# Kernel tuning notes

Hardware: AMD Instinct MI355X
Metric: run time of the kernel (lower is better)

The kernel has to match this reference:

```python
import jax, jax.numpy as jnp
import numpy as np

B, T, I, E, K, J = 4, 4096, 1024, 16, 512, 1024


def setup_inputs() -> dict:
    key = jax.random.key(0)
    k1, k2, k3 = jax.random.split(key, 3)
    X = jax.random.normal(k1, (B, T, I), dtype=jnp.float32)
    ind = jax.random.randint(k2, (B, E, K), 0, T, dtype=jnp.int64)
    bound = 1.0 / np.sqrt(J)
    W = jax.random.uniform(k3, (E, I, J), dtype=jnp.float32, minval=-bound, maxval=bound)
    return {"X": X, "ind": ind, "W": W}


def reference(X, ind, W):
    Bs, Ts, Is = X.shape
    _, Es, Ks = ind.shape
    # gather tokens per expert: [B, E*K, I] -> [B, E, K, I]
    idx = ind.reshape(Bs, Es * Ks)
    Xg = jnp.take_along_axis(X, idx[:, :, None], axis=1).reshape(Bs, Es, Ks, Is)
    # per-expert GEMM
    Y = jnp.einsum('beki,eij->bekj', Xg, W)
    return Y
```

## Files before the change

kernel.cpp:

```cpp
#include <hip/hip_runtime.h>
#include <cstdint>
#include <cstddef>


typedef float    floatx4 __attribute__((ext_vector_type(4)));
typedef _Float16 half8   __attribute__((ext_vector_type(8)));

constexpr int Bc = 4, Tc = 4096, Ic = 1024, Ec = 16, Kc = 512, Jc = 1024;
constexpr int BM = 256, BN = 256, BK = 64, NT = 512;

__device__ __forceinline__ void async16(const void* g, void* l) {
  __builtin_amdgcn_global_load_lds(
      (const __attribute__((address_space(1))) uint32_t*)g,
      (__attribute__((address_space(3))) uint32_t*)l, 16, 0, 0);
}

__global__ void cvt_x_kernel(const float* __restrict__ X, _Float16* __restrict__ Xh, int n8) {
  int i = blockIdx.x * blockDim.x + threadIdx.x;
  int stride = gridDim.x * blockDim.x;
  for (; i < n8; i += stride) {
    floatx4 v0 = ((const floatx4*)X)[2 * i];
    floatx4 v1 = ((const floatx4*)X)[2 * i + 1];
    half8 h;
    h[0] = (_Float16)v0.x; h[1] = (_Float16)v0.y; h[2] = (_Float16)v0.z; h[3] = (_Float16)v0.w;
    h[4] = (_Float16)v1.x; h[5] = (_Float16)v1.y; h[6] = (_Float16)v1.z; h[7] = (_Float16)v1.w;
    ((half8*)Xh)[i] = h;
  }
}

__global__ void cvt_w_kernel(const float* __restrict__ W, _Float16* __restrict__ WT) {
  __shared__ float tile[64][65];
  int bid = blockIdx.x;
  int e  = bid >> 8;
  int i0 = ((bid >> 4) & 15) * 64;
  int j0 = (bid & 15) * 64;
  int tid = threadIdx.x;
  int r  = tid >> 4;
  int c4 = tid & 15;
  const float* src = W + ((size_t)e << 20) + (size_t)i0 * Jc + j0;
#pragma unroll
  for (int s = 0; s < 4; s++) {
    int rr = r + s * 16;
    floatx4 v = *(const floatx4*)(src + (size_t)rr * Jc + c4 * 4);
    tile[rr][c4 * 4 + 0] = v.x; tile[rr][c4 * 4 + 1] = v.y;
    tile[rr][c4 * 4 + 2] = v.z; tile[rr][c4 * 4 + 3] = v.w;
  }
  __syncthreads();
  int jj = tid >> 2;
  int ig = tid & 3;
  half8 hv0, hv1;
#pragma unroll
  for (int q = 0; q < 8; q++) hv0[q] = (_Float16)tile[ig * 16 + q][jj];
#pragma unroll
  for (int q = 0; q < 8; q++) hv1[q] = (_Float16)tile[ig * 16 + 8 + q][jj];
  _Float16* dst = WT + ((size_t)e << 20) + (size_t)(j0 + jj) * Ic + i0 + ig * 16;
  ((half8*)dst)[0] = hv0;
  ((half8*)dst)[1] = hv1;
}

__global__ __launch_bounds__(NT, 2) void gemm_kernel(
    const int* __restrict__ ind32,
    const _Float16* __restrict__ Xh, const _Float16* __restrict__ WT,
    float* __restrict__ Y) {
  __shared__ alignas(16) unsigned char smem[(BM + BN) * BK * 2];
  _Float16* As = (_Float16*)smem;
  _Float16* Bs = (_Float16*)(smem + BM * BK * 2);
  float* lbuf = (float*)smem;
  __shared__ int rowid[BM];
  __shared__ int is64_s;

  const int tid = threadIdx.x;
  const int bid = blockIdx.x;
  const int x = bid & 7, s = (bid >> 3) & 7, chunk = bid >> 6;
  const int g = chunk * 8 + x;
  const int e = g >> 2, nt = g & 3;
  const int b = s >> 1, mt = s & 1;
  const int be = b * Ec + e;
  const int k0 = mt * BM;
  const int j0 = nt * BN;

  if (tid == 0) {
    int orv = 0;
    for (int q = 1; q < 256; q += 2) orv |= ind32[q];
    is64_s = (orv == 0) ? 1 : 0;
  }
  __syncthreads();
  if (tid < BM) {
    int idx = be * Kc + k0 + tid;
    rowid[tid] = is64_s ? ind32[2 * idx] : ind32[idx];
  }
  __syncthreads();

  const int lane = tid & 63;
  const int wave = tid >> 6;
  const int wmb = (wave >> 2) * 128;
  const int wnb = (wave & 3) * 64;
  const int quad = lane >> 4;
  const int tr = lane & 15;
  const int t7 = tr & 7;
  const int lr = lane >> 3;
  const int cst = lane & 7;
  const int cdat = cst ^ lr;

  const _Float16* aptr[4];
  const _Float16* bptr[4];
#pragma unroll
  for (int q = 0; q < 4; q++) {
    const int rowA = (wave * 4 + q) * 8 + lr;
    aptr[q] = Xh + ((size_t)b * Tc + rowid[rowA]) * Ic + cdat * 8;
    bptr[q] = WT + ((size_t)e * Jc + j0 + rowA) * Ic + cdat * 8;
  }

  floatx4 acc[8][4];
#pragma unroll
  for (int mi = 0; mi < 8; mi++)
#pragma unroll
    for (int ni = 0; ni < 4; ni++) acc[mi][ni] = {0.f, 0.f, 0.f, 0.f};

  for (int kk = 0; kk < Ic; kk += BK) {
#pragma unroll
    for (int q = 0; q < 4; q++)
      async16(aptr[q] + kk, &As[(wave * 4 + q) * 512]);
#pragma unroll
    for (int q = 0; q < 4; q++)
      async16(bptr[q] + kk, &Bs[(wave * 4 + q) * 512]);
    __syncthreads();

#pragma unroll
    for (int ks = 0; ks < 2; ks++) {
      const int cofs = ((ks * 4 + quad) ^ t7) * 8;
      half8 bf[4];
#pragma unroll
      for (int ni = 0; ni < 4; ni++)
        bf[ni] = *(const half8*)&Bs[(wnb + ni * 16 + tr) * 64 + cofs];
#pragma unroll
      for (int mi = 0; mi < 8; mi++) {
        half8 af = *(const half8*)&As[(wmb + mi * 16 + tr) * 64 + cofs];
#pragma unroll
        for (int ni = 0; ni < 4; ni++)
          acc[mi][ni] = __builtin_amdgcn_mfma_f32_16x16x32_f16(af, bf[ni], acc[mi][ni], 0, 0, 0);
      }
    }
    __syncthreads();
  }

  constexpr int LST = 257;
  float* Yb = Y + (size_t)be * Kc * Jc;
#pragma unroll
  for (int pass = 0; pass < 8; pass++) {
    if ((wave >> 2) == (pass >> 2)) {
#pragma unroll
      for (int h = 0; h < 2; h++) {
        const int mi = (pass & 3) * 2 + h;
        const int rr = h * 16 + quad * 4;
#pragma unroll
        for (int ni = 0; ni < 4; ni++) {
          const int col = wnb + ni * 16 + tr;
#pragma unroll
          for (int r = 0; r < 4; r++)
            lbuf[(rr + r) * LST + col] = acc[mi][ni][r];
        }
      }
    }
    __syncthreads();
#pragma unroll
    for (int it = 0; it < 4; it++) {
      const int idx = tid + it * NT;
      const int rr = idx >> 6, c4 = idx & 63;
      floatx4 v = *(const floatx4*)&lbuf[rr * LST + c4 * 4];
      *(floatx4*)&Yb[(size_t)(k0 + pass * 32 + rr) * Jc + j0 + c4 * 4] = v;
    }
    __syncthreads();
  }
}

extern "C" void kernel_launch(void* const* d_in, const int* in_sizes, int n_in,
                              void* d_out, int out_size, void* d_ws, size_t ws_size,
                              hipStream_t stream) {
  const float* X = (const float*)d_in[0];
  const int* ind = (const int*)d_in[1];
  const float* W = (const float*)d_in[2];
  float* Y = (float*)d_out;

  const size_t nx = (size_t)Bc * Tc * Ic;
  _Float16* Xh = (_Float16*)d_ws;
  _Float16* WT = Xh + nx;

  cvt_x_kernel<<<2048, 256, 0, stream>>>(X, Xh, (int)(nx / 8));
  cvt_w_kernel<<<Ec * 256, 256, 0, stream>>>(W, WT);
  const int gemm_grid = (Bc * Ec) * (Kc / BM) * (Jc / BN) * 1;
  gemm_kernel<<<gemm_grid, NT, 0, stream>>>(ind, Xh, WT, Y);
}
```

Measured before the change: 325.2 us.

## Software-pipeline GEMM K-loop with 4-stage LDS ring and merge convert kernels

Restructures the GEMM main loop into a multi-stage async LDS pipeline: each BK=64 tile is split into two 32-wide half-stages in a 4-slot ring, with prefetches issued two stages ahead, split barriers, explicit vmcnt waits and raised MFMA priority. LDS use grows from 64KB to 128KB per block, which may reduce occupancy from the requested two blocks per CU. The X and W fp16 conversion kernels are merged into one launch, and the int64 index detection uses a wave ballot instead of a serial loop.

```diff
diff --git a/kernel.cpp b/kernel.cpp
--- a/kernel.cpp
+++ b/kernel.cpp
@@ -8,6 +8,9 @@
 
 constexpr int Bc = 4, Tc = 4096, Ic = 1024, Ec = 16, Kc = 512, Jc = 1024;
 constexpr int BM = 256, BN = 256, BK = 64, NT = 512;
+constexpr int NKT = Ic / BK;
+constexpr int UNIT = 16384;
+constexpr int BOFF = 4 * UNIT;
 
 __device__ __forceinline__ void async16(const void* g, void* l) {
   __builtin_amdgcn_global_load_lds(
@@ -15,28 +18,30 @@
       (__attribute__((address_space(3))) uint32_t*)l, 16, 0, 0);
 }
 
-__global__ void cvt_x_kernel(const float* __restrict__ X, _Float16* __restrict__ Xh, int n8) {
-  int i = blockIdx.x * blockDim.x + threadIdx.x;
-  int stride = gridDim.x * blockDim.x;
-  for (; i < n8; i += stride) {
-    floatx4 v0 = ((const floatx4*)X)[2 * i];
-    floatx4 v1 = ((const floatx4*)X)[2 * i + 1];
-    half8 h;
-    h[0] = (_Float16)v0.x; h[1] = (_Float16)v0.y; h[2] = (_Float16)v0.z; h[3] = (_Float16)v0.w;
-    h[4] = (_Float16)v1.x; h[5] = (_Float16)v1.y; h[6] = (_Float16)v1.z; h[7] = (_Float16)v1.w;
-    ((half8*)Xh)[i] = h;
-  }
-}
-
-__global__ void cvt_w_kernel(const float* __restrict__ W, _Float16* __restrict__ WT) {
+__global__ void cvt_kernel(const float* __restrict__ X, _Float16* __restrict__ Xh, int n8,
+                           const float* __restrict__ W, _Float16* __restrict__ WT) {
   __shared__ float tile[64][65];
-  int bid = blockIdx.x;
-  int e  = bid >> 8;
-  int i0 = ((bid >> 4) & 15) * 64;
-  int j0 = (bid & 15) * 64;
-  int tid = threadIdx.x;
-  int r  = tid >> 4;
-  int c4 = tid & 15;
+  const int bidx = blockIdx.x;
+  if (bidx >= Ec * 256) {
+    int i = (bidx - Ec * 256) * blockDim.x + threadIdx.x;
+    const int stride = 2048 * blockDim.x;
+    for (; i < n8; i += stride) {
+      floatx4 v0 = ((const floatx4*)X)[2 * i];
+      floatx4 v1 = ((const floatx4*)X)[2 * i + 1];
+      half8 h;
+      h[0] = (_Float16)v0.x; h[1] = (_Float16)v0.y; h[2] = (_Float16)v0.z; h[3] = (_Float16)v0.w;
+      h[4] = (_Float16)v1.x; h[5] = (_Float16)v1.y; h[6] = (_Float16)v1.z; h[7] = (_Float16)v1.w;
+      ((half8*)Xh)[i] = h;
+    }
+    return;
+  }
+  const int bid = bidx;
+  const int e  = bid >> 8;
+  const int i0 = ((bid >> 4) & 15) * 64;
+  const int j0 = (bid & 15) * 64;
+  const int tid = threadIdx.x;
+  const int r  = tid >> 4;
+  const int c4 = tid & 15;
   const float* src = W + ((size_t)e << 20) + (size_t)i0 * Jc + j0;
 #pragma unroll
   for (int s = 0; s < 4; s++) {
@@ -46,8 +51,8 @@
     tile[rr][c4 * 4 + 2] = v.z; tile[rr][c4 * 4 + 3] = v.w;
   }
   __syncthreads();
-  int jj = tid >> 2;
-  int ig = tid & 3;
+  const int jj = tid >> 2;
+  const int ig = tid & 3;
   half8 hv0, hv1;
 #pragma unroll
   for (int q = 0; q < 8; q++) hv0[q] = (_Float16)tile[ig * 16 + q][jj];
@@ -62,12 +67,11 @@
     const int* __restrict__ ind32,
     const _Float16* __restrict__ Xh, const _Float16* __restrict__ WT,
     float* __restrict__ Y) {
-  __shared__ alignas(16) unsigned char smem[(BM + BN) * BK * 2];
-  _Float16* As = (_Float16*)smem;
-  _Float16* Bs = (_Float16*)(smem + BM * BK * 2);
-  float* lbuf = (float*)smem;
+  __shared__ alignas(16) unsigned char smem[8 * UNIT];
   __shared__ int rowid[BM];
   __shared__ int is64_s;
+  float* lbuf = (float*)smem;
+  char* smemc = (char*)smem;
 
   const int tid = threadIdx.x;
   const int bid = blockIdx.x;
@@ -79,10 +83,10 @@
   const int k0 = mt * BM;
   const int j0 = nt * BN;
 
-  if (tid == 0) {
-    int orv = 0;
-    for (int q = 1; q < 256; q += 2) orv |= ind32[q];
-    is64_s = (orv == 0) ? 1 : 0;
+  if (tid < 64) {
+    int v = ind32[2 * tid + 1];
+    unsigned long long m = __ballot(v != 0);
+    if (tid == 0) is64_s = (m == 0ULL) ? 1 : 0;
   }
   __syncthreads();
   if (tid < BM) {
@@ -97,18 +101,35 @@
   const int wnb = (wave & 3) * 64;
   const int quad = lane >> 4;
   const int tr = lane & 15;
-  const int t7 = tr & 7;
-  const int lr = lane >> 3;
-  const int cst = lane & 7;
-  const int cdat = cst ^ lr;
-
-  const _Float16* aptr[4];
-  const _Float16* bptr[4];
-#pragma unroll
-  for (int q = 0; q < 4; q++) {
-    const int rowA = (wave * 4 + q) * 8 + lr;
-    aptr[q] = Xh + ((size_t)b * Tc + rowid[rowA]) * Ic + cdat * 8;
-    bptr[q] = WT + ((size_t)e * Jc + j0 + rowA) * Ic + cdat * 8;
+
+  const _Float16* aSrc[2];
+  const _Float16* bSrc[2];
+#pragma unroll
+  for (int q = 0; q < 2; q++) {
+    const int sl = wave * 128 + q * 64 + lane;
+    const int r2 = sl >> 3, p = sl & 7;
+    const int pos = p ^ (r2 & 7);
+    const int r = 2 * r2 + (pos >> 2);
+    const int c = pos & 3;
+    aSrc[q] = Xh + ((size_t)b * Tc + rowid[r]) * Ic + c * 8;
+    bSrc[q] = WT + ((size_t)e * Jc + j0 + r) * Ic + c * 8;
+  }
+  const int wdst = wave * 2048;
+
+  int offA[2][4], offB[4];
+#pragma unroll
+  for (int mh = 0; mh < 2; mh++)
+#pragma unroll
+    for (int mi = 0; mi < 4; mi++) {
+      const int R = wmb + mh * 64 + mi * 16 + tr;
+      const int r2 = R >> 1;
+      offA[mh][mi] = r2 * 128 + ((((R & 1) << 2) | quad) ^ (r2 & 7)) * 16;
+    }
+#pragma unroll
+  for (int ni = 0; ni < 4; ni++) {
+    const int R = wnb + ni * 16 + tr;
+    const int r2 = R >> 1;
+    offB[ni] = r2 * 128 + ((((R & 1) << 2) | quad) ^ (r2 & 7)) * 16;
   }
 
   floatx4 acc[8][4];
@@ -117,32 +138,63 @@
 #pragma unroll
     for (int ni = 0; ni < 4; ni++) acc[mi][ni] = {0.f, 0.f, 0.f, 0.f};
 
-  for (int kk = 0; kk < Ic; kk += BK) {
-#pragma unroll
-    for (int q = 0; q < 4; q++)
-      async16(aptr[q] + kk, &As[(wave * 4 + q) * 512]);
-#pragma unroll
-    for (int q = 0; q < 4; q++)
-      async16(bptr[q] + kk, &Bs[(wave * 4 + q) * 512]);
-    __syncthreads();
-
-#pragma unroll
-    for (int ks = 0; ks < 2; ks++) {
-      const int cofs = ((ks * 4 + quad) ^ t7) * 8;
-      half8 bf[4];
-#pragma unroll
-      for (int ni = 0; ni < 4; ni++)
-        bf[ni] = *(const half8*)&Bs[(wnb + ni * 16 + tr) * 64 + cofs];
-#pragma unroll
-      for (int mi = 0; mi < 8; mi++) {
-        half8 af = *(const half8*)&As[(wmb + mi * 16 + tr) * 64 + cofs];
-#pragma unroll
-        for (int ni = 0; ni < 4; ni++)
-          acc[mi][ni] = __builtin_amdgcn_mfma_f32_16x16x32_f16(af, bf[ni], acc[mi][ni], 0, 0, 0);
-      }
-    }
-    __syncthreads();
-  }
+#define STAGE_A(TT, KS) do { \
+    char* d_ = smemc + ((2 * (TT) + (KS)) & 3) * UNIT + wdst; \
+    async16(aSrc[0] + (TT) * 64 + (KS) * 32, d_); \
+    async16(aSrc[1] + (TT) * 64 + (KS) * 32, d_ + 1024); \
+  } while (0)
+#define STAGE_B(TT, KS) do { \
+    char* d_ = smemc + BOFF + ((2 * (TT) + (KS)) & 3) * UNIT + wdst; \
+    async16(bSrc[0] + (TT) * 64 + (KS) * 32, d_); \
+    async16(bSrc[1] + (TT) * 64 + (KS) * 32, d_ + 1024); \
+  } while (0)
+
+#define PHASE(SK, MH, STAGE_STMT, CLOSE_STMT) do { \
+    const char* Ab_ = smemc + (SK) * UNIT; \
+    const char* Bb_ = smemc + BOFF + (SK) * UNIT; \
+    half8 af_[4], bf_[4]; \
+    _Pragma("unroll") \
+    for (int mi_ = 0; mi_ < 4; mi_++) af_[mi_] = *(const half8*)(Ab_ + offA[MH][mi_]); \
+    _Pragma("unroll") \
+    for (int ni_ = 0; ni_ < 4; ni_++) bf_[ni_] = *(const half8*)(Bb_ + offB[ni_]); \
+    STAGE_STMT \
+    __builtin_amdgcn_s_barrier(); \
+    asm volatile("s_waitcnt lgkmcnt(0)" ::: "memory"); \
+    __builtin_amdgcn_sched_barrier(0); \
+    __builtin_amdgcn_s_setprio(1); \
+    _Pragma("unroll") \
+    for (int mi_ = 0; mi_ < 4; mi_++) \
+      _Pragma("unroll") \
+      for (int ni_ = 0; ni_ < 4; ni_++) \
+        acc[(MH) * 4 + mi_][ni_] = __builtin_amdgcn_mfma_f32_16x16x32_f16( \
+            af_[mi_], bf_[ni_], acc[(MH) * 4 + mi_][ni_], 0, 0, 0); \
+    __builtin_amdgcn_s_setprio(0); \
+    CLOSE_STMT \
+    __builtin_amdgcn_s_barrier(); \
+  } while (0)
+
+  STAGE_A(0, 0); STAGE_B(0, 0);
+  STAGE_A(0, 1); STAGE_B(0, 1);
+  STAGE_A(1, 0); STAGE_B(1, 0);
+  asm volatile("s_waitcnt vmcnt(4)" ::: "memory");
+  __builtin_amdgcn_s_barrier();
+
+#pragma unroll 2
+  for (int t = 0; t < NKT; t++) {
+    const int sk0 = (2 * t) & 3;
+    const int sk1 = sk0 + 1;
+    const bool f1 = (t + 1 < NKT);
+    const bool f2 = (t + 2 < NKT);
+    PHASE(sk0, 0, { if (f1) STAGE_A(t + 1, 1); }, {});
+    PHASE(sk0, 1, { if (f1) STAGE_B(t + 1, 1); }, {});
+    PHASE(sk1, 0, { if (f2) STAGE_A(t + 2, 0); }, {});
+    PHASE(sk1, 1, { if (f2) STAGE_B(t + 2, 0); },
+          { if (t == NKT - 2) { asm volatile("s_waitcnt vmcnt(0)" ::: "memory"); }
+            else if (t < NKT - 2) { asm volatile("s_waitcnt vmcnt(4)" ::: "memory"); } });
+  }
+#undef PHASE
+#undef STAGE_A
+#undef STAGE_B
 
   constexpr int LST = 257;
   float* Yb = Y + (size_t)be * Kc * Jc;
@@ -186,8 +238,7 @@
   _Float16* Xh = (_Float16*)d_ws;
   _Float16* WT = Xh + nx;
 
-  cvt_x_kernel<<<2048, 256, 0, stream>>>(X, Xh, (int)(nx / 8));
-  cvt_w_kernel<<<Ec * 256, 256, 0, stream>>>(W, WT);
-  const int gemm_grid = (Bc * Ec) * (Kc / BM) * (Jc / BN) * 1;
+  cvt_kernel<<<Ec * 256 + 2048, 256, 0, stream>>>(X, Xh, (int)(nx / 8), W, WT);
+  const int gemm_grid = (Bc * Ec) * (Kc / BM) * (Jc / BN);
   gemm_kernel<<<gemm_grid, NT, 0, stream>>>(ind, Xh, WT, Y);
 }
```

Result: faster. 314.4 us (-3.3%).
